# Optimization experiments

Hardware: AMD Instinct MI355X
Metric: run time of the kernel (lower is better)

## Reference

```python
import jax, jax.numpy as jnp
import numpy as np

B, S, BD, AD, H, NITER = 16, 512, 768, 768, 12, 3  # batch, seq, bert_dim, attention_dim, heads, c_c_Attention_num
DH = AD // H
SCALE = float(np.sqrt(BD))  # note: original scales by sqrt(bert_dim), not head dim


def setup_inputs() -> dict:
    key = jax.random.key(0)
    ks = jax.random.split(key, 12)
    sd = 0.02
    return {
        "sequence1": jax.random.normal(ks[0], (B, S, BD), dtype=jnp.float32),
        "sequence2": jax.random.normal(ks[1], (B, S, BD), dtype=jnp.float32),
        # first-layer projections (bias=False), torch Linear weight layout [out, in]
        "Wq": jax.random.normal(ks[2], (AD, BD), dtype=jnp.float32) * sd,
        "Wk": jax.random.normal(ks[3], (AD, BD), dtype=jnp.float32) * sd,
        "Wv": jax.random.normal(ks[4], (AD, BD), dtype=jnp.float32) * sd,
        # later-layer projections (with bias), stacked over layer_num-1 = 2 layers
        "Wq1": jax.random.normal(ks[5], (2, AD, AD), dtype=jnp.float32) * sd,
        "bq1": jax.random.normal(ks[6], (2, AD), dtype=jnp.float32) * sd,
        "Wk1": jax.random.normal(ks[7], (2, AD, AD), dtype=jnp.float32) * sd,
        "bk1": jax.random.normal(ks[8], (2, AD), dtype=jnp.float32) * sd,
        "Wv1": jax.random.normal(ks[9], (2, AD, AD), dtype=jnp.float32) * sd,
        "bv1": jax.random.normal(ks[10], (2, AD), dtype=jnp.float32) * sd,
    }


def _attention(s1, s2, Wq, bq, Wk, bk, Wv, bv):
    # dropout is identity in eval mode
    q = s1 @ Wq.T + bq  # [B,S,AD]
    k = s2 @ Wk.T + bk
    v = s2 @ Wv.T + bv
    # torch.split along feature dim then stack on dim 0 == reshape to heads
    qh = q.reshape(B, S, H, DH)
    kh = k.reshape(B, S, H, DH)
    vh = v.reshape(B, S, H, DH)
    scores = jnp.einsum("bqhd,bkhd->hbqk", qh, kh)  # [H,B,S,S]
    scores = jax.nn.softmax(jnp.tanh(scores) / SCALE, axis=3)
    ctx = jnp.einsum("hbqk,bkhd->bqhd", scores, vh).reshape(B, S, AD)
    return ctx, scores


def reference(sequence1, sequence2, Wq, Wk, Wv, Wq1, bq1, Wk1, bk1, Wv1, bv1):
    s1, s2 = sequence1, sequence2
    ctx, sc = None, None
    for i in range(NITER):
        if i == 0:
            ctx, sc = _attention(s1, s2, Wq, 0.0, Wk, 0.0, Wv, 0.0)
        else:
            j = i - 1
            ctx, sc = _attention(s1, s2, Wq1[j], bq1[j], Wk1[j], bk1[j], Wv1[j], bv1[j])
        s1 = ctx
        s2 = ctx
    return ctx, ctx, sc
```

## Files before the change

kernel.cpp:

```cpp
#include <hip/hip_runtime.h>
#include <stdint.h>

typedef unsigned short u16;
typedef unsigned int u32;

typedef __bf16 bf16x8 __attribute__((ext_vector_type(8)));
typedef float f32x4 __attribute__((ext_vector_type(4)));

#define NQ 6291456
#define NW 589824
#define INV_SCALE 0.03608439182435161f
#define LOG2E2 2.885390081777927f

__device__ __forceinline__ u16 f2bf(float f) {
    u32 u = __float_as_uint(f);
    u32 r = (u + 0x7fffu + ((u >> 16) & 1u)) >> 16;
    return (u16)r;
}

__device__ __forceinline__ float score_p(float s) {
    float e  = exp2f(LOG2E2 * s);
    float th = 1.f - __fdividef(2.f, e + 1.f);
    float a  = th * INV_SCALE;
    return fmaf(a, fmaf(a, fmaf(a, 0.16666667f, 0.5f), 1.f), 1.f);
}

__device__ __forceinline__ void gload_lds16(const void* g, void* l) {
    __builtin_amdgcn_global_load_lds(
        (const __attribute__((address_space(1))) char*)(uintptr_t)g,
        (__attribute__((address_space(3))) char*)(uintptr_t)l, 16, 0, 0);
}

__device__ __forceinline__ f32x4 mfma16(bf16x8 a, bf16x8 b, f32x4 c) {
    return __builtin_amdgcn_mfma_f32_16x16x32_bf16(a, b, c, 0, 0, 0);
}

#define LDS_FENCE() asm volatile("s_waitcnt lgkmcnt(0)" ::: "memory")

struct CvtArgs {
    const float* src[8];
    u16* dst[8];
    int blk_start[8];
    int n4[8];
};

__global__ __launch_bounds__(256) void cvt_multi(CvtArgs a)
{
    const int bid = blockIdx.x;
    int seg = 0;
#pragma unroll
    for (int s = 1; s < 8; ++s) seg += (bid >= a.blk_start[s]);
    const int i = (bid - a.blk_start[seg]) * 256 + threadIdx.x;
    if (i < a.n4[seg]) {
        float4 v = ((const float4*)a.src[seg])[i];
        ushort4 o;
        o.x = f2bf(v.x); o.y = f2bf(v.y); o.z = f2bf(v.z); o.w = f2bf(v.w);
        ((ushort4*)a.dst[seg])[i] = o;
    }
}

__global__ __launch_bounds__(256, 2) void proj_gemm(
    const u16* __restrict__ A0, const u16* __restrict__ A1,
    const u16* __restrict__ Wq, const u16* __restrict__ Wk, const u16* __restrict__ Wv,
    const float* __restrict__ bq, const float* __restrict__ bk, const float* __restrict__ bv,
    u16* __restrict__ oq, u16* __restrict__ ok, u16* __restrict__ ov)
{
    __shared__ u16 sA[2][8192];
    __shared__ u16 sB[2][8192];

    const int z = blockIdx.z;
    const u16* A       = (z == 0) ? A0 : A1;
    const u16* W       = (z == 0) ? Wq : ((z == 1) ? Wk : Wv);
    const float* bias  = (z == 0) ? bq : ((z == 1) ? bk : bv);
    u16* out           = (z == 0) ? oq : ((z == 1) ? ok : ov);

    const int tid = threadIdx.x;
    const int wave = tid >> 6, lane = tid & 63;
    const int m0 = blockIdx.x * 128, n0 = blockIdx.y * 128;
    const int wrow = wave >> 1, wcol = wave & 1;
    const int lr = lane & 15, lg = lane >> 4;

    const int Lb0 = wave * 4096;
    const int srow = (Lb0 + lane * 16) >> 7;
    const int ssl = (lane & 7);

    f32x4 acc[4][4];
#pragma unroll
    for (int mi = 0; mi < 4; ++mi)
#pragma unroll
        for (int ni = 0; ni < 4; ++ni)
            acc[mi][ni] = (f32x4){0.f, 0.f, 0.f, 0.f};

#define STAGE(buf, k0)                                                          \
    {                                                                           \
        _Pragma("unroll")                                                       \
        for (int i = 0; i < 4; ++i) {                                           \
            const int row = srow + i * 8;                                       \
            const int sc16 = ssl ^ (row & 7);                                   \
            gload_lds16(A + (size_t)(m0 + row) * 768 + (k0) + sc16 * 8,         \
                        (char*)sA[buf] + Lb0 + i * 1024);                       \
            gload_lds16(W + (size_t)(n0 + row) * 768 + (k0) + sc16 * 8,         \
                        (char*)sB[buf] + Lb0 + i * 1024);                       \
        }                                                                       \
    }

    STAGE(0, 0);
    __syncthreads();

    for (int ks = 0; ks < 12; ++ks) {
        const int cur = ks & 1;
        if (ks < 11) STAGE(cur ^ 1, (ks + 1) * 64);
#pragma unroll
        for (int kk = 0; kk < 2; ++kk) {
            bf16x8 af[4], bfr[4];
#pragma unroll
            for (int t = 0; t < 4; ++t) {
                const int ar = wrow * 64 + t * 16 + lr;
                const int ac = (kk * 4 + lg) ^ (ar & 7);
                af[t] = *(const bf16x8*)((const char*)sA[cur] + ar * 128 + ac * 16);
                const int br = wcol * 64 + t * 16 + lr;
                const int bc = (kk * 4 + lg) ^ (br & 7);
                bfr[t] = *(const bf16x8*)((const char*)sB[cur] + br * 128 + bc * 16);
            }
#pragma unroll
            for (int mi = 0; mi < 4; ++mi)
#pragma unroll
                for (int ni = 0; ni < 4; ++ni)
                    acc[mi][ni] = mfma16(af[mi], bfr[ni], acc[mi][ni]);
        }
        __syncthreads();
    }
#undef STAGE

    float bvv[4] = {0.f, 0.f, 0.f, 0.f};
    if (bias) {
#pragma unroll
        for (int ni = 0; ni < 4; ++ni)
            bvv[ni] = bias[n0 + wcol * 64 + ni * 16 + lr];
    }
#pragma unroll
    for (int mi = 0; mi < 4; ++mi) {
#pragma unroll
        for (int ni = 0; ni < 4; ++ni) {
#pragma unroll
            for (int r = 0; r < 4; ++r) {
                const int rowM = m0 + wrow * 64 + mi * 16 + lg * 4 + r;
                const int colN = n0 + wcol * 64 + ni * 16 + lr;
                out[(size_t)rowM * 768 + colN] = f2bf(acc[mi][ni][r] + bvv[ni]);
            }
        }
    }
}

__global__ __launch_bounds__(256) void vtrans(const u16* __restrict__ v, u16* __restrict__ vT)
{
    __shared__ u16 t[64][80];
    const int blk = blockIdx.x;
    const int b = blk / 96, h = (blk / 8) % 12, st = blk & 7;
    const int tid = threadIdx.x;

    const u16* src = v + (size_t)(b * 512 + st * 64) * 768 + h * 64;
#pragma unroll
    for (int p = 0; p < 2; ++p) {
        const int srow = p * 32 + (tid >> 3), dp = tid & 7;
        uint4 d = *(const uint4*)(src + (size_t)srow * 768 + dp * 8);
        *(uint4*)&t[srow][dp * 8] = d;
    }
    __syncthreads();
    u16* dst = vT + (size_t)((b * 12 + h) * 64) * 512 + st * 64;
#pragma unroll
    for (int p = 0; p < 2; ++p) {
        const int drow = p * 32 + (tid >> 3), sp = tid & 7;
        union { u16 u[8]; uint4 v4; } o;
#pragma unroll
        for (int j = 0; j < 8; ++j) o.u[j] = t[sp * 8 + j][drow];
        *(uint4*)(dst + (size_t)drow * 512 + sp * 8) = o.v4;
    }
}

__global__ __launch_bounds__(256, 4) void attn_stream(
    const u16* __restrict__ q, const u16* __restrict__ k, const u16* __restrict__ vT,
    u16* __restrict__ ctx)
{
    __shared__ u16 sS[4][2][640];

    const int blk = blockIdx.x;
    const int bh = blk % 192, qc = blk / 192;
    const int b = bh / 12, h = bh % 12;
    const int tid = threadIdx.x, wave = tid >> 6, lane = tid & 63;
    const int q0 = qc * 64 + wave * 16;
    const int lr = lane & 15, lg = lane >> 4;

    const u16* qbase = q + (size_t)(b * 512 + q0 + lr) * 768 + h * 64 + lg * 8;
    bf16x8 aq0 = *(const bf16x8*)(qbase);
    bf16x8 aq1 = *(const bf16x8*)(qbase + 32);

    const u16* kbase = k + (size_t)(b * 512 + lr) * 768 + h * 64 + lg * 8;
    const u16* vbase = vT + (size_t)((b * 12 + h) * 64 + lr) * 512 + lg * 8;

    char* const myS0 = (char*)sS[wave][0];
    const int rdoff = lr * 80 + ((lg * 16) ^ ((lr & 3) << 4));

    float psum[4] = {0.f, 0.f, 0.f, 0.f};
    f32x4 o[4];
#pragma unroll
    for (int dt = 0; dt < 4; ++dt) o[dt] = (f32x4){0.f, 0.f, 0.f, 0.f};

    for (int w = 0; w < 16; ++w) {
        char* myS = myS0 + (w & 1) * 1280;
        const u16* kb = kbase + (size_t)w * 32 * 768;
        f32x4 s4a = (f32x4){0.f, 0.f, 0.f, 0.f};
        f32x4 s4b = (f32x4){0.f, 0.f, 0.f, 0.f};
        s4a = mfma16(aq0, *(const bf16x8*)kb, s4a);
        s4a = mfma16(aq1, *(const bf16x8*)(kb + 32), s4a);
        const u16* kb2 = kb + 16 * 768;
        s4b = mfma16(aq0, *(const bf16x8*)kb2, s4b);
        s4b = mfma16(aq1, *(const bf16x8*)(kb2 + 32), s4b);

#pragma unroll
        for (int c = 0; c < 2; ++c) {
#pragma unroll
            for (int r = 0; r < 4; ++r) {
                const float s = c ? s4b[r] : s4a[r];
                const float p = score_p(s);
                psum[r] += p;
                const int row = lg * 4 + r;
                const int byte = row * 80 + (((c * 16 + lr) * 2) ^ ((r & 3) << 4));
                *(u16*)(myS + byte) = f2bf(p);
            }
        }
        LDS_FENCE();
        bf16x8 pa = *(const bf16x8*)(myS + rdoff);
#pragma unroll
        for (int dt = 0; dt < 4; ++dt) {
            bf16x8 vb = *(const bf16x8*)(vbase + (size_t)dt * 16 * 512 + w * 32);
            o[dt] = mfma16(pa, vb, o[dt]);
        }
    }

#pragma unroll
    for (int r = 0; r < 4; ++r) {
        psum[r] += __shfl_xor(psum[r], 1);
        psum[r] += __shfl_xor(psum[r], 2);
        psum[r] += __shfl_xor(psum[r], 4);
        psum[r] += __shfl_xor(psum[r], 8);
    }
    float inv[4];
#pragma unroll
    for (int r = 0; r < 4; ++r) inv[r] = 1.f / psum[r];

#pragma unroll
    for (int dt = 0; dt < 4; ++dt) {
#pragma unroll
        for (int r = 0; r < 4; ++r) {
            const size_t gi = (size_t)(b * 512 + q0 + lg * 4 + r) * 768 + h * 64 + dt * 16 + lr;
            ctx[gi] = f2bf(o[dt][r] * inv[r]);
        }
    }
}

__global__ __launch_bounds__(256, 4) void attn_final(
    const u16* __restrict__ q, const u16* __restrict__ k, const u16* __restrict__ vT,
    float* __restrict__ ctxf, float* __restrict__ sc)
{
    __shared__ u16 sS[4][2][640];

    const int blk = blockIdx.x;
    const int bh = blk % 192, qc = blk / 192;
    const int b = bh / 12, h = bh % 12;
    const int tid = threadIdx.x, wave = tid >> 6, lane = tid & 63;
    const int q0 = qc * 64 + wave * 16;
    const int lr = lane & 15, lg = lane >> 4;

    const u16* qbase = q + (size_t)(b * 512 + q0 + lr) * 768 + h * 64 + lg * 8;
    bf16x8 aq0 = *(const bf16x8*)(qbase);
    bf16x8 aq1 = *(const bf16x8*)(qbase + 32);

    const u16* kbase = k + (size_t)(b * 512 + lr) * 768 + h * 64 + lg * 8;
    const u16* vbase = vT + (size_t)((b * 12 + h) * 64 + lr) * 512 + lg * 8;

    char* const myS0 = (char*)sS[wave][0];
    const int rdoff = lr * 80 + ((lg * 16) ^ ((lr & 3) << 4));

    float psum[4] = {0.f, 0.f, 0.f, 0.f};
    for (int w = 0; w < 16; ++w) {
        const u16* kb = kbase + (size_t)w * 32 * 768;
        f32x4 s4a = (f32x4){0.f, 0.f, 0.f, 0.f};
        f32x4 s4b = (f32x4){0.f, 0.f, 0.f, 0.f};
        s4a = mfma16(aq0, *(const bf16x8*)kb, s4a);
        s4a = mfma16(aq1, *(const bf16x8*)(kb + 32), s4a);
        const u16* kb2 = kb + 16 * 768;
        s4b = mfma16(aq0, *(const bf16x8*)kb2, s4b);
        s4b = mfma16(aq1, *(const bf16x8*)(kb2 + 32), s4b);
#pragma unroll
        for (int r = 0; r < 4; ++r)
            psum[r] += score_p(s4a[r]) + score_p(s4b[r]);
    }
#pragma unroll
    for (int r = 0; r < 4; ++r) {
        psum[r] += __shfl_xor(psum[r], 1);
        psum[r] += __shfl_xor(psum[r], 2);
        psum[r] += __shfl_xor(psum[r], 4);
        psum[r] += __shfl_xor(psum[r], 8);
    }
    float inv[4];
#pragma unroll
    for (int r = 0; r < 4; ++r) inv[r] = 1.f / psum[r];

    f32x4 o[4];
#pragma unroll
    for (int dt = 0; dt < 4; ++dt) o[dt] = (f32x4){0.f, 0.f, 0.f, 0.f};

    float* scb = sc + ((size_t)((h * 16 + b) * 512 + q0)) * 512;

    for (int w = 0; w < 16; ++w) {
        char* myS = myS0 + (w & 1) * 1280;
        const u16* kb = kbase + (size_t)w * 32 * 768;
        f32x4 s4a = (f32x4){0.f, 0.f, 0.f, 0.f};
        f32x4 s4b = (f32x4){0.f, 0.f, 0.f, 0.f};
        s4a = mfma16(aq0, *(const bf16x8*)kb, s4a);
        s4a = mfma16(aq1, *(const bf16x8*)(kb + 32), s4a);
        const u16* kb2 = kb + 16 * 768;
        s4b = mfma16(aq0, *(const bf16x8*)kb2, s4b);
        s4b = mfma16(aq1, *(const bf16x8*)(kb2 + 32), s4b);

#pragma unroll
        for (int c = 0; c < 2; ++c) {
#pragma unroll
            for (int r = 0; r < 4; ++r) {
                const float s = c ? s4b[r] : s4a[r];
                const float p = score_p(s);
                const int row = lg * 4 + r;
                scb[(size_t)row * 512 + w * 32 + c * 16 + lr] = p * inv[r];
                const int byte = row * 80 + (((c * 16 + lr) * 2) ^ ((r & 3) << 4));
                *(u16*)(myS + byte) = f2bf(p);
            }
        }
        LDS_FENCE();
        bf16x8 pa = *(const bf16x8*)(myS + rdoff);
#pragma unroll
        for (int dt = 0; dt < 4; ++dt) {
            bf16x8 vb = *(const bf16x8*)(vbase + (size_t)dt * 16 * 512 + w * 32);
            o[dt] = mfma16(pa, vb, o[dt]);
        }
    }

#pragma unroll
    for (int dt = 0; dt < 4; ++dt) {
#pragma unroll
        for (int r = 0; r < 4; ++r) {
            const float val = o[dt][r] * inv[r];
            const size_t gi = (size_t)(b * 512 + q0 + lg * 4 + r) * 768 + h * 64 + dt * 16 + lr;
            ctxf[gi] = val;
            ctxf[gi + (size_t)NQ] = val;
        }
    }
}

extern "C" void kernel_launch(void* const* d_in, const int* in_sizes, int n_in,
                              void* d_out, int out_size, void* d_ws, size_t ws_size,
                              hipStream_t stream)
{
    if (n_in < 11) return;
    const float* seq1 = (const float*)d_in[0];
    const float* seq2 = (const float*)d_in[1];
    const float* Wq  = (const float*)d_in[2];
    const float* Wk  = (const float*)d_in[3];
    const float* Wv  = (const float*)d_in[4];
    const float* Wq1 = (const float*)d_in[5];
    const float* bq1 = (const float*)d_in[6];
    const float* Wk1 = (const float*)d_in[7];
    const float* bk1 = (const float*)d_in[8];
    const float* Wv1 = (const float*)d_in[9];
    const float* bv1 = (const float*)d_in[10];

    if (ws_size < ((size_t)7 * NQ + 9 * NW) * 2) return;
    u16* ws   = (u16*)d_ws;
    u16* q    = ws;
    u16* kk   = ws + (size_t)NQ;
    u16* vv   = ws + (size_t)2 * NQ;
    u16* vT   = ws + (size_t)3 * NQ;
    u16* ctx  = ws + (size_t)4 * NQ;
    u16* bs1  = ws + (size_t)5 * NQ;
    u16* bs2  = ws + (size_t)6 * NQ;
    u16* bWq  = ws + (size_t)7 * NQ;
    u16* bWk  = bWq  + (size_t)NW;
    u16* bWv  = bWk  + (size_t)NW;
    u16* bWq1 = bWv  + (size_t)NW;
    u16* bWk1 = bWq1 + (size_t)2 * NW;
    u16* bWv1 = bWk1 + (size_t)2 * NW;

    float* out = (float*)d_out;

    CvtArgs ca;
    const float* srcs[8] = {seq1, seq2, Wq, Wk, Wv, Wq1, Wk1, Wv1};
    u16* dsts[8] = {bs1, bs2, bWq, bWk, bWv, bWq1, bWk1, bWv1};
    const int n4s[8] = {NQ/4, NQ/4, NW/4, NW/4, NW/4, NW/2, NW/2, NW/2};
    int acc_blk = 0;
    for (int s = 0; s < 8; ++s) {
        ca.src[s] = srcs[s]; ca.dst[s] = dsts[s]; ca.n4[s] = n4s[s];
        ca.blk_start[s] = acc_blk;
        acc_blk += (n4s[s] + 255) / 256;
    }
    cvt_multi<<<acc_blk, 256, 0, stream>>>(ca);

    dim3 pgrid(64, 6, 3);

    proj_gemm<<<pgrid, 256, 0, stream>>>(bs1, bs2, bWq, bWk, bWv,
                                         nullptr, nullptr, nullptr, q, kk, vv);
    vtrans<<<1536, 256, 0, stream>>>(vv, vT);
    attn_stream<<<1536, 256, 0, stream>>>(q, kk, vT, ctx);

    proj_gemm<<<pgrid, 256, 0, stream>>>(ctx, ctx, bWq1, bWk1, bWv1,
                                         bq1, bk1, bv1, q, kk, vv);
    vtrans<<<1536, 256, 0, stream>>>(vv, vT);
    attn_stream<<<1536, 256, 0, stream>>>(q, kk, vT, ctx);

    proj_gemm<<<pgrid, 256, 0, stream>>>(ctx, ctx, bWq1 + (size_t)NW, bWk1 + (size_t)NW,
                                         bWv1 + (size_t)NW,
                                         bq1 + 768, bk1 + 768, bv1 + 768, q, kk, vv);
    vtrans<<<1536, 256, 0, stream>>>(vv, vT);
    attn_final<<<1536, 256, 0, stream>>>(q, kk, vT, out, out + (size_t)2 * NQ);
}
```

Measured before the change: 473.7 us.

## Single-pass final attention with deferred score normalization kernel

The final attention kernel drops its separate row-sum pass over QK^T. Instead it accumulates row sums during the PV loop and stores unnormalized bf16 probabilities and per-row inverse sums to workspace. A new elementwise kernel then writes normalized fp32 scores with vectorized stores. This trades recomputation of scores for extra memory traffic through the bf16 buffer, and it lowers score precision to bf16-rounded values.

```diff
diff --git a/kernel.cpp b/kernel.cpp
--- a/kernel.cpp
+++ b/kernel.cpp
@@ -9,6 +9,8 @@
 
 #define NQ 6291456
 #define NW 589824
+#define NSC 50331648
+#define NR 98304
 #define INV_SCALE 0.03608439182435161f
 #define LOG2E2 2.885390081777927f
 
@@ -259,9 +261,9 @@
     }
 }
 
-__global__ __launch_bounds__(256, 4) void attn_final(
+__global__ __launch_bounds__(256, 4) void attn_final_s(
     const u16* __restrict__ q, const u16* __restrict__ k, const u16* __restrict__ vT,
-    float* __restrict__ ctxf, float* __restrict__ sc)
+    float* __restrict__ ctxf, u16* __restrict__ pbuf, float* __restrict__ invs)
 {
     __shared__ u16 sS[4][2][640];
 
@@ -282,36 +284,12 @@
     char* const myS0 = (char*)sS[wave][0];
     const int rdoff = lr * 80 + ((lg * 16) ^ ((lr & 3) << 4));
 
+    u16* prow = pbuf + ((size_t)((h * 16 + b) * 512 + q0 + lr)) * 512 + lg * 8;
+
     float psum[4] = {0.f, 0.f, 0.f, 0.f};
-    for (int w = 0; w < 16; ++w) {
-        const u16* kb = kbase + (size_t)w * 32 * 768;
-        f32x4 s4a = (f32x4){0.f, 0.f, 0.f, 0.f};
-        f32x4 s4b = (f32x4){0.f, 0.f, 0.f, 0.f};
-        s4a = mfma16(aq0, *(const bf16x8*)kb, s4a);
-        s4a = mfma16(aq1, *(const bf16x8*)(kb + 32), s4a);
-        const u16* kb2 = kb + 16 * 768;
-        s4b = mfma16(aq0, *(const bf16x8*)kb2, s4b);
-        s4b = mfma16(aq1, *(const bf16x8*)(kb2 + 32), s4b);
-#pragma unroll
-        for (int r = 0; r < 4; ++r)
-            psum[r] += score_p(s4a[r]) + score_p(s4b[r]);
-    }
-#pragma unroll
-    for (int r = 0; r < 4; ++r) {
-        psum[r] += __shfl_xor(psum[r], 1);
-        psum[r] += __shfl_xor(psum[r], 2);
-        psum[r] += __shfl_xor(psum[r], 4);
-        psum[r] += __shfl_xor(psum[r], 8);
-    }
-    float inv[4];
-#pragma unroll
-    for (int r = 0; r < 4; ++r) inv[r] = 1.f / psum[r];
-
     f32x4 o[4];
 #pragma unroll
     for (int dt = 0; dt < 4; ++dt) o[dt] = (f32x4){0.f, 0.f, 0.f, 0.f};
-
-    float* scb = sc + ((size_t)((h * 16 + b) * 512 + q0)) * 512;
 
     for (int w = 0; w < 16; ++w) {
         char* myS = myS0 + (w & 1) * 1280;
@@ -330,19 +308,37 @@
             for (int r = 0; r < 4; ++r) {
                 const float s = c ? s4b[r] : s4a[r];
                 const float p = score_p(s);
+                psum[r] += p;
                 const int row = lg * 4 + r;
-                scb[(size_t)row * 512 + w * 32 + c * 16 + lr] = p * inv[r];
                 const int byte = row * 80 + (((c * 16 + lr) * 2) ^ ((r & 3) << 4));
                 *(u16*)(myS + byte) = f2bf(p);
             }
         }
         LDS_FENCE();
         bf16x8 pa = *(const bf16x8*)(myS + rdoff);
+        *(bf16x8*)(prow + w * 32) = pa;
 #pragma unroll
         for (int dt = 0; dt < 4; ++dt) {
             bf16x8 vb = *(const bf16x8*)(vbase + (size_t)dt * 16 * 512 + w * 32);
             o[dt] = mfma16(pa, vb, o[dt]);
         }
+    }
+
+#pragma unroll
+    for (int r = 0; r < 4; ++r) {
+        psum[r] += __shfl_xor(psum[r], 1);
+        psum[r] += __shfl_xor(psum[r], 2);
+        psum[r] += __shfl_xor(psum[r], 4);
+        psum[r] += __shfl_xor(psum[r], 8);
+    }
+    float inv[4];
+#pragma unroll
+    for (int r = 0; r < 4; ++r) inv[r] = 1.f / psum[r];
+
+    if (lr == 0) {
+        const int ibase = (h * 16 + b) * 512 + q0 + lg * 4;
+#pragma unroll
+        for (int r = 0; r < 4; ++r) invs[ibase + r] = inv[r];
     }
 
 #pragma unroll
@@ -355,6 +351,25 @@
             ctxf[gi + (size_t)NQ] = val;
         }
     }
+}
+
+__global__ __launch_bounds__(256) void score_norm(
+    const u16* __restrict__ pbuf, const float* __restrict__ invs,
+    float* __restrict__ sc)
+{
+    const int i = blockIdx.x * 256 + threadIdx.x;
+    const int row = i >> 6;
+    const float inv = invs[row];
+    const size_t base = ((size_t)row * 512) + (i & 63) * 8;
+    bf16x8 p = *(const bf16x8*)(pbuf + base);
+    float4 o0, o1;
+    o0.x = (float)p[0] * inv; o0.y = (float)p[1] * inv;
+    o0.z = (float)p[2] * inv; o0.w = (float)p[3] * inv;
+    o1.x = (float)p[4] * inv; o1.y = (float)p[5] * inv;
+    o1.z = (float)p[6] * inv; o1.w = (float)p[7] * inv;
+    float* dst = sc + base;
+    *(float4*)dst = o0;
+    *(float4*)(dst + 4) = o1;
 }
 
 extern "C" void kernel_launch(void* const* d_in, const int* in_sizes, int n_in,
@@ -374,7 +389,8 @@
     const float* Wv1 = (const float*)d_in[9];
     const float* bv1 = (const float*)d_in[10];
 
-    if (ws_size < ((size_t)7 * NQ + 9 * NW) * 2) return;
+    const size_t need = ((size_t)7 * NQ + 9 * NW + NSC) * 2 + (size_t)NR * 4;
+    if (ws_size < need) return;
     u16* ws   = (u16*)d_ws;
     u16* q    = ws;
     u16* kk   = ws + (size_t)NQ;
@@ -389,6 +405,8 @@
     u16* bWq1 = bWv  + (size_t)NW;
     u16* bWk1 = bWq1 + (size_t)2 * NW;
     u16* bWv1 = bWk1 + (size_t)2 * NW;
+    u16* pbuf = bWv1 + (size_t)2 * NW;
+    float* invs = (float*)(pbuf + (size_t)NSC);
 
     float* out = (float*)d_out;
 
@@ -420,5 +438,6 @@
                                          bWv1 + (size_t)NW,
                                          bq1 + 768, bk1 + 768, bv1 + 768, q, kk, vv);
     vtrans<<<1536, 256, 0, stream>>>(vv, vT);
-    attn_final<<<1536, 256, 0, stream>>>(q, kk, vT, out, out + (size_t)2 * NQ);
-}
+    attn_final_s<<<1536, 256, 0, stream>>>(q, kk, vT, out, pbuf, invs);
+    score_norm<<<NSC / 8 / 256, 256, 0, stream>>>(pbuf, invs, out + (size_t)2 * NQ);
+}
```

Result: no change. 472.9 us (-0.2%).

## Fuse final attention into a single pass and use 32x32 MFMA in projection GEMM

Applied to the files above, without the earlier changes.

The final attention kernel no longer runs a separate pass to compute softmax row sums. It now accumulates the sums during the P·V loop and keeps the bf16 probability fragments in registers. Afterwards it normalizes them and writes the score matrix as row-contiguous float4 stores instead of scattered scalar stores. This removes the duplicated QK^T and exp work and makes the large score output coalesced. The trade-offs are that the emitted scores are now derived from bf16-rounded probabilities, and register pressure rises. Separately, the projection GEMM switches from 16x16x32 to 32x32x16 MFMA tiles, which means fewer instructions and LDS fragment loads per wave.

```diff
diff --git a/kernel.cpp b/kernel.cpp
--- a/kernel.cpp
+++ b/kernel.cpp
@@ -6,6 +6,7 @@
 
 typedef __bf16 bf16x8 __attribute__((ext_vector_type(8)));
 typedef float f32x4 __attribute__((ext_vector_type(4)));
+typedef float f32x16 __attribute__((ext_vector_type(16)));
 
 #define NQ 6291456
 #define NW 589824
@@ -33,6 +34,9 @@
 
 __device__ __forceinline__ f32x4 mfma16(bf16x8 a, bf16x8 b, f32x4 c) {
     return __builtin_amdgcn_mfma_f32_16x16x32_bf16(a, b, c, 0, 0, 0);
+}
+__device__ __forceinline__ f32x16 mfma32(bf16x8 a, bf16x8 b, f32x16 c) {
+    return __builtin_amdgcn_mfma_f32_32x32x16_bf16(a, b, c, 0, 0, 0);
 }
 
 #define LDS_FENCE() asm volatile("s_waitcnt lgkmcnt(0)" ::: "memory")
@@ -78,18 +82,20 @@
     const int wave = tid >> 6, lane = tid & 63;
     const int m0 = blockIdx.x * 128, n0 = blockIdx.y * 128;
     const int wrow = wave >> 1, wcol = wave & 1;
-    const int lr = lane & 15, lg = lane >> 4;
+    const int l31 = lane & 31, l5 = lane >> 5;
 
     const int Lb0 = wave * 4096;
     const int srow = (Lb0 + lane * 16) >> 7;
     const int ssl = (lane & 7);
 
-    f32x4 acc[4][4];
-#pragma unroll
-    for (int mi = 0; mi < 4; ++mi)
-#pragma unroll
-        for (int ni = 0; ni < 4; ++ni)
-            acc[mi][ni] = (f32x4){0.f, 0.f, 0.f, 0.f};
+    f32x16 acc[2][2];
+#pragma unroll
+    for (int mi = 0; mi < 2; ++mi)
+#pragma unroll
+        for (int ni = 0; ni < 2; ++ni)
+#pragma unroll
+            for (int e = 0; e < 16; ++e)
+                acc[mi][ni][e] = 0.f;
 
 #define STAGE(buf, k0)                                                          \
     {                                                                           \
@@ -111,42 +117,41 @@
         const int cur = ks & 1;
         if (ks < 11) STAGE(cur ^ 1, (ks + 1) * 64);
 #pragma unroll
-        for (int kk = 0; kk < 2; ++kk) {
-            bf16x8 af[4], bfr[4];
-#pragma unroll
-            for (int t = 0; t < 4; ++t) {
-                const int ar = wrow * 64 + t * 16 + lr;
-                const int ac = (kk * 4 + lg) ^ (ar & 7);
-                af[t] = *(const bf16x8*)((const char*)sA[cur] + ar * 128 + ac * 16);
-                const int br = wcol * 64 + t * 16 + lr;
-                const int bc = (kk * 4 + lg) ^ (br & 7);
-                bfr[t] = *(const bf16x8*)((const char*)sB[cur] + br * 128 + bc * 16);
+        for (int ks4 = 0; ks4 < 4; ++ks4) {
+            bf16x8 af[2], bfr[2];
+#pragma unroll
+            for (int t = 0; t < 2; ++t) {
+                const int ar = wrow * 64 + t * 32 + l31;
+                const int sa = (ks4 * 2 + l5) ^ (ar & 7);
+                af[t] = *(const bf16x8*)((const char*)sA[cur] + ar * 128 + sa * 16);
+                const int br = wcol * 64 + t * 32 + l31;
+                const int sb = (ks4 * 2 + l5) ^ (br & 7);
+                bfr[t] = *(const bf16x8*)((const char*)sB[cur] + br * 128 + sb * 16);
             }
 #pragma unroll
-            for (int mi = 0; mi < 4; ++mi)
-#pragma unroll
-                for (int ni = 0; ni < 4; ++ni)
-                    acc[mi][ni] = mfma16(af[mi], bfr[ni], acc[mi][ni]);
+            for (int mi = 0; mi < 2; ++mi)
+#pragma unroll
+                for (int ni = 0; ni < 2; ++ni)
+                    acc[mi][ni] = mfma32(af[mi], bfr[ni], acc[mi][ni]);
         }
         __syncthreads();
     }
 #undef STAGE
 
-    float bvv[4] = {0.f, 0.f, 0.f, 0.f};
+    float bvv[2] = {0.f, 0.f};
     if (bias) {
-#pragma unroll
-        for (int ni = 0; ni < 4; ++ni)
-            bvv[ni] = bias[n0 + wcol * 64 + ni * 16 + lr];
-    }
-#pragma unroll
-    for (int mi = 0; mi < 4; ++mi) {
-#pragma unroll
-        for (int ni = 0; ni < 4; ++ni) {
-#pragma unroll
-            for (int r = 0; r < 4; ++r) {
-                const int rowM = m0 + wrow * 64 + mi * 16 + lg * 4 + r;
-                const int colN = n0 + wcol * 64 + ni * 16 + lr;
-                out[(size_t)rowM * 768 + colN] = f2bf(acc[mi][ni][r] + bvv[ni]);
+        bvv[0] = bias[n0 + wcol * 64 + l31];
+        bvv[1] = bias[n0 + wcol * 64 + 32 + l31];
+    }
+#pragma unroll
+    for (int mi = 0; mi < 2; ++mi) {
+#pragma unroll
+        for (int ni = 0; ni < 2; ++ni) {
+#pragma unroll
+            for (int reg = 0; reg < 16; ++reg) {
+                const int rowM = m0 + wrow * 64 + mi * 32 + (reg & 3) + 8 * (reg >> 2) + 4 * l5;
+                const int colN = n0 + wcol * 64 + ni * 32 + l31;
+                out[(size_t)rowM * 768 + colN] = f2bf(acc[mi][ni][reg] + bvv[ni]);
             }
         }
     }
@@ -259,7 +264,7 @@
     }
 }
 
-__global__ __launch_bounds__(256, 4) void attn_final(
+__global__ __launch_bounds__(256, 4) void attn_final_s(
     const u16* __restrict__ q, const u16* __restrict__ k, const u16* __restrict__ vT,
     float* __restrict__ ctxf, float* __restrict__ sc)
 {
@@ -283,36 +288,12 @@
     const int rdoff = lr * 80 + ((lg * 16) ^ ((lr & 3) << 4));
 
     float psum[4] = {0.f, 0.f, 0.f, 0.f};
-    for (int w = 0; w < 16; ++w) {
-        const u16* kb = kbase + (size_t)w * 32 * 768;
-        f32x4 s4a = (f32x4){0.f, 0.f, 0.f, 0.f};
-        f32x4 s4b = (f32x4){0.f, 0.f, 0.f, 0.f};
-        s4a = mfma16(aq0, *(const bf16x8*)kb, s4a);
-        s4a = mfma16(aq1, *(const bf16x8*)(kb + 32), s4a);
-        const u16* kb2 = kb + 16 * 768;
-        s4b = mfma16(aq0, *(const bf16x8*)kb2, s4b);
-        s4b = mfma16(aq1, *(const bf16x8*)(kb2 + 32), s4b);
-#pragma unroll
-        for (int r = 0; r < 4; ++r)
-            psum[r] += score_p(s4a[r]) + score_p(s4b[r]);
-    }
-#pragma unroll
-    for (int r = 0; r < 4; ++r) {
-        psum[r] += __shfl_xor(psum[r], 1);
-        psum[r] += __shfl_xor(psum[r], 2);
-        psum[r] += __shfl_xor(psum[r], 4);
-        psum[r] += __shfl_xor(psum[r], 8);
-    }
-    float inv[4];
-#pragma unroll
-    for (int r = 0; r < 4; ++r) inv[r] = 1.f / psum[r];
-
     f32x4 o[4];
 #pragma unroll
     for (int dt = 0; dt < 4; ++dt) o[dt] = (f32x4){0.f, 0.f, 0.f, 0.f};
-
-    float* scb = sc + ((size_t)((h * 16 + b) * 512 + q0)) * 512;
-
+    bf16x8 pfrag[16];
+
+#pragma unroll
     for (int w = 0; w < 16; ++w) {
         char* myS = myS0 + (w & 1) * 1280;
         const u16* kb = kbase + (size_t)w * 32 * 768;
@@ -330,19 +311,52 @@
             for (int r = 0; r < 4; ++r) {
                 const float s = c ? s4b[r] : s4a[r];
                 const float p = score_p(s);
+                psum[r] += p;
                 const int row = lg * 4 + r;
-                scb[(size_t)row * 512 + w * 32 + c * 16 + lr] = p * inv[r];
                 const int byte = row * 80 + (((c * 16 + lr) * 2) ^ ((r & 3) << 4));
                 *(u16*)(myS + byte) = f2bf(p);
             }
         }
         LDS_FENCE();
         bf16x8 pa = *(const bf16x8*)(myS + rdoff);
+        pfrag[w] = pa;
 #pragma unroll
         for (int dt = 0; dt < 4; ++dt) {
             bf16x8 vb = *(const bf16x8*)(vbase + (size_t)dt * 16 * 512 + w * 32);
             o[dt] = mfma16(pa, vb, o[dt]);
         }
+    }
+
+#pragma unroll
+    for (int r = 0; r < 4; ++r) {
+        psum[r] += __shfl_xor(psum[r], 1);
+        psum[r] += __shfl_xor(psum[r], 2);
+        psum[r] += __shfl_xor(psum[r], 4);
+        psum[r] += __shfl_xor(psum[r], 8);
+    }
+    float inv[4];
+#pragma unroll
+    for (int r = 0; r < 4; ++r) inv[r] = 1.f / psum[r];
+
+    const int srcl = (lr >> 2) << 4;
+    const float v0 = __shfl(inv[0], srcl);
+    const float v1 = __shfl(inv[1], srcl);
+    const float v2 = __shfl(inv[2], srcl);
+    const float v3 = __shfl(inv[3], srcl);
+    const int sel = lr & 3;
+    const float invlr = (sel == 0) ? v0 : (sel == 1) ? v1 : (sel == 2) ? v2 : v3;
+
+    float* scrow = sc + ((size_t)((h * 16 + b) * 512 + q0 + lr)) * 512 + lg * 8;
+#pragma unroll
+    for (int w = 0; w < 16; ++w) {
+        const bf16x8 pf = pfrag[w];
+        float4 o0, o1;
+        o0.x = (float)pf[0] * invlr; o0.y = (float)pf[1] * invlr;
+        o0.z = (float)pf[2] * invlr; o0.w = (float)pf[3] * invlr;
+        o1.x = (float)pf[4] * invlr; o1.y = (float)pf[5] * invlr;
+        o1.z = (float)pf[6] * invlr; o1.w = (float)pf[7] * invlr;
+        *(float4*)(scrow + w * 32) = o0;
+        *(float4*)(scrow + w * 32 + 4) = o1;
     }
 
 #pragma unroll
@@ -420,5 +434,5 @@
                                          bWv1 + (size_t)NW,
                                          bq1 + 768, bk1 + 768, bv1 + 768, q, kk, vv);
     vtrans<<<1536, 256, 0, stream>>>(vv, vT);
-    attn_final<<<1536, 256, 0, stream>>>(q, kk, vT, out, out + (size_t)2 * NQ);
-}
+    attn_final_s<<<1536, 256, 0, stream>>>(q, kk, vT, out, out + (size_t)2 * NQ);
+}
```

Measured after the change: 465.7 us. No clear change (-1.7%).
